# Kernel tuning notes

Measured on AMD Instinct MI355X. Metric: run time of the kernel, lower is better.

Reference implementation:

```python
import jax, jax.numpy as jnp
import numpy as np
from jax import lax

B, N, K, D = 16, 64, 20, 4096
DI, DO, H, L = 1024, 1024, 1024, 2


def setup_inputs() -> dict:
    key = jax.random.key(0)
    ks = jax.random.split(key, 16)
    s = 0.02
    x = jax.random.normal(ks[0], (B, N, K, D), dtype=jnp.float32)
    W_img = jax.random.normal(ks[1], (D, DI), dtype=jnp.float32) * s
    b_img = jnp.zeros((DI,), jnp.float32)
    W_obj = jax.random.normal(ks[2], (D, DO), dtype=jnp.float32) * s
    b_obj = jnp.zeros((DO,), jnp.float32)
    W_obj2 = jax.random.normal(ks[3], (DO, DO), dtype=jnp.float32) * s
    b_obj2 = jnp.zeros((DO,), jnp.float32)
    W_attn_h = jax.random.normal(ks[4], (H, DO), dtype=jnp.float32) * s  # hidden_lin, no bias
    W_attn_j = jax.random.normal(ks[5], (DO, 1), dtype=jnp.float32) * s  # joint_lin, no bias
    W_ih0 = jax.random.normal(ks[6], (4 * H, DI + DO), dtype=jnp.float32) * s
    W_hh0 = jax.random.normal(ks[7], (4 * H, H), dtype=jnp.float32) * s
    b0 = jnp.zeros((4 * H,), jnp.float32)  # b_ih + b_hh combined
    W_ih1 = jax.random.normal(ks[8], (4 * H, H), dtype=jnp.float32) * s
    W_hh1 = jax.random.normal(ks[9], (4 * H, H), dtype=jnp.float32) * s
    b1 = jnp.zeros((4 * H,), jnp.float32)
    W_out = jax.random.normal(ks[10], (H, 1), dtype=jnp.float32) * s
    b_out = jnp.zeros((1,), jnp.float32)
    return dict(x=x, W_img=W_img, b_img=b_img, W_obj=W_obj, b_obj=b_obj,
                W_obj2=W_obj2, b_obj2=b_obj2, W_attn_h=W_attn_h, W_attn_j=W_attn_j,
                W_ih0=W_ih0, W_hh0=W_hh0, b0=b0, W_ih1=W_ih1, W_hh1=W_hh1, b1=b1,
                W_out=W_out, b_out=b_out)


def _lstm_cell(xin, h, c, W_ih, W_hh, b):
    # PyTorch gate order: i, f, g, o
    g = xin @ W_ih.T + h @ W_hh.T + b
    i, f, gg, o = jnp.split(g, 4, axis=-1)
    c_new = jax.nn.sigmoid(f) * c + jax.nn.sigmoid(i) * jnp.tanh(gg)
    h_new = jax.nn.sigmoid(o) * jnp.tanh(c_new)
    return h_new, c_new


def reference(x, W_img, b_img, W_obj, b_obj, W_obj2, b_obj2, W_attn_h, W_attn_j,
              W_ih0, W_hh0, b0, W_ih1, W_hh1, b1, W_out, b_out):
    # obj_mask: (B,N,K-1,1)
    obj_mask = jnp.sum(x[:, :, 1:], axis=-1, keepdims=True)
    img_feat = x[:, :, 0, :] @ W_img + b_img                       # (B,N,DI)
    obj_feat = (x[:, :, 1:, :] @ W_obj + b_obj) * obj_mask          # (B,N,K-1,DO)
    a = obj_feat @ W_obj2 + b_obj2                                  # (B,N,K-1,DO)

    # move frame axis first for scan
    a_t = jnp.moveaxis(a, 1, 0)          # (N,B,K-1,DO)
    img_t = jnp.moveaxis(img_feat, 1, 0)  # (N,B,DI)
    m_t = jnp.moveaxis(obj_mask, 1, 0)    # (N,B,K-1,1)

    h0 = jnp.zeros((L, x.shape[0], H), x.dtype)
    c0 = jnp.zeros((L, x.shape[0], H), x.dtype)

    def step(carry, inp):
        h, c = carry
        a_f, img_f, m_f = inp
        # Fattn: alpha = softmax(joint_lin(tanh(hidden_lin(h_prev) + a)) * mask) over objects
        e = jnp.tanh((h[-1] @ W_attn_h)[:, None, :] + a_f)          # (B,K-1,DO)
        scores = (e @ W_attn_j) * m_f                                # (B,K-1,1)
        alphas = jax.nn.softmax(scores, axis=1)                      # over K-1
        w_obj = jnp.sum(a_f * alphas, axis=1)                        # (B,DO)
        fusion = jnp.concatenate([img_f, w_obj], axis=-1)            # (B,DI+DO)
        h1, c1 = _lstm_cell(fusion, h[0], c[0], W_ih0, W_hh0, b0)
        h2, c2 = _lstm_cell(h1, h[1], c[1], W_ih1, W_hh1, b1)
        pred = jax.nn.sigmoid(h2 @ W_out + b_out)                    # (B,1)
        return (jnp.stack([h1, h2]), jnp.stack([c1, c2])), (alphas[..., 0], pred)

    _, (all_alphas, all_preds) = lax.scan(step, (h0, c0), (a_t, img_t, m_t))
    return all_alphas, all_preds  # (N,B,K-1), (N,B,1)
```

## Files before the change

kernel.cpp:

```cpp
#include <hip/hip_runtime.h>
#include <cmath>

constexpr int B_  = 16;
constexpr int N_  = 64;
constexpr int K_  = 20;
constexpr int KM1 = 19;
constexpr int D_  = 4096;
constexpr int DO_ = 1024;
constexpr int H_  = 1024;
constexpr int G4_ = 4096;

typedef unsigned short u16;
typedef unsigned int   u32;
typedef __attribute__((ext_vector_type(8))) short bf16x8;
typedef __attribute__((ext_vector_type(4))) float f32x4;

typedef const void __attribute__((address_space(1)))* gas1_t;
typedef void __attribute__((address_space(3)))* las3_t;

static __device__ __forceinline__ void gll16(const void* g, void* l) {
  __builtin_amdgcn_global_load_lds((gas1_t)g, (las3_t)l, 16, 0, 0);
}

static __device__ __forceinline__ float sigmoidf_(float x) {
  return 1.0f / (1.0f + expf(-x));
}

static __device__ __forceinline__ u16 bf16rne(float f) {
  u32 u = __float_as_uint(f);
  return (u16)((u + 0x7fffu + ((u >> 16) & 1u)) >> 16);
}

static __device__ __forceinline__ float block_reduce_sum256(float v, float* red) {
  #pragma unroll
  for (int off = 32; off > 0; off >>= 1) v += __shfl_down(v, off);
  const int wid = threadIdx.x >> 6;
  if ((threadIdx.x & 63) == 0) red[wid] = v;
  __syncthreads();
  const float r = red[0] + red[1] + red[2] + red[3];
  __syncthreads();
  return r;
}

__global__ __launch_bounds__(256) void mask_kernel(const float* __restrict__ x,
                                                   float* __restrict__ mask) {
  const int r = blockIdx.x;
  const int g = r / KM1, kk = r - g * KM1;
  const float4* xp = (const float4*)(x + ((size_t)g * K_ + 1 + kk) * D_);
  float v = 0.f;
  #pragma unroll
  for (int it = 0; it < 4; ++it) {
    const float4 t = xp[threadIdx.x + it * 256];
    v += (t.x + t.y) + (t.z + t.w);
  }
  __shared__ float red[4];
  const float s = block_reduce_sum256(v, red);
  if (threadIdx.x == 0) mask[r] = s;
}

__global__ __launch_bounds__(256) void conv_kernel(
    const float* __restrict__ src, const int ld, const int cols,
    u16* __restrict__ oh, u16* __restrict__ ol)
{
  const int id = blockIdx.x * 256 + threadIdx.x;
  const int r = id / (cols >> 2), q = id - r * (cols >> 2);
  const float4 v = *(const float4*)(src + (size_t)r * ld + q * 4);
  const float vv[4] = {v.x, v.y, v.z, v.w};
  u16 h[4], lo[4];
  #pragma unroll
  for (int j = 0; j < 4; ++j) {
    h[j] = bf16rne(vv[j]);
    lo[j] = bf16rne(vv[j] - __uint_as_float((u32)h[j] << 16));
  }
  const size_t o = (size_t)r * cols + q * 4;
  *(ushort4*)(oh + o) = make_ushort4(h[0], h[1], h[2], h[3]);
  *(ushort4*)(ol + o) = make_ushort4(lo[0], lo[1], lo[2], lo[3]);
}

__global__ __launch_bounds__(256) void tconv_kernel(
    const float* __restrict__ src, const int R, const int C,
    u16* __restrict__ oh, u16* __restrict__ ol)
{
  __shared__ float st[64][68];
  const int t = threadIdx.x;
  const int r0 = blockIdx.y * 64, c0 = blockIdx.x * 64;
  const int lr = t >> 4, lc4 = (t & 15) * 4;
  #pragma unroll
  for (int i = 0; i < 4; ++i) {
    const float4 v = *(const float4*)(src + (size_t)(r0 + lr + 16 * i) * C + c0 + lc4);
    st[lr + 16 * i][lc4 + 0] = v.x; st[lr + 16 * i][lc4 + 1] = v.y;
    st[lr + 16 * i][lc4 + 2] = v.z; st[lr + 16 * i][lc4 + 3] = v.w;
  }
  __syncthreads();
  #pragma unroll
  for (int i = 0; i < 4; ++i) {
    const int s = t + 256 * i;
    const int c = s & 63, rq = s >> 6;
    u16 h[4], lo[4];
    #pragma unroll
    for (int j = 0; j < 4; ++j) {
      const float f = st[rq * 4 + j][c];
      h[j] = bf16rne(f);
      lo[j] = bf16rne(f - __uint_as_float((u32)h[j] << 16));
    }
    const size_t o = (size_t)(c0 + c) * R + r0 + rq * 4;
    *(ushort4*)(oh + o) = make_ushort4(h[0], h[1], h[2], h[3]);
    *(ushort4*)(ol + o) = make_ushort4(lo[0], lo[1], lo[2], lo[3]);
  }
}

__global__ __launch_bounds__(256) void bf_kernel(
    const float* __restrict__ b1, const float* __restrict__ W2, float* __restrict__ bf)
{
  const int n = blockIdx.x * 256 + threadIdx.x;
  float acc = 0.f;
  for (int j = 0; j < 1024; ++j) acc = fmaf(b1[j], W2[(size_t)j * 1024 + n], acc);
  bf[n] = acc;
}

template<int AMODE, int EPI>
__global__ __launch_bounds__(256, 2) void mfma_gemm(
    const float* __restrict__ Af,
    const u16* __restrict__ Ah, const u16* __restrict__ Al,
    const u16* __restrict__ Bh, const u16* __restrict__ Bl,
    const float* __restrict__ bias, const float* __restrict__ bias2,
    const float* __restrict__ scale,
    float* __restrict__ Cf, u16* __restrict__ Coh, u16* __restrict__ Col,
    const int Kk, const int Nn)
{
  __shared__ alignas(16) char sm[32768];
  const int t = threadIdx.x;
  const int m0 = blockIdx.x * 128, n0 = blockIdx.y * 128;
  const int w = t >> 6, l = t & 63;
  const int wm = w >> 1, wn = w & 1;

  const int srow = t >> 3;
  const int sc16 = (t & 7) * 16;

  const u16* bsrc[4]; int bdst[4];
  #pragma unroll
  for (int i = 0; i < 4; ++i) {
    const int row = srow + 32 * i;
    const int clog = sc16 ^ ((row & 7) << 4);
    const u16* base = (clog & 64) ? Bl : Bh;
    bsrc[i] = base + (size_t)(n0 + row) * Kk + ((clog & 63) >> 1);
    bdst[i] = 16384 + row * 128 + sc16;
  }

  const float* aptr[4]; int awhi[4], awlo[4];
  const u16* asrc[4]; int adst[4];
  if (AMODE == 0) {
    #pragma unroll
    for (int i = 0; i < 4; ++i) {
      const int row = srow + 32 * i;
      const int clog = sc16 ^ ((row & 7) << 4);
      const u16* base = (clog & 64) ? Al : Ah;
      asrc[i] = base + (size_t)(m0 + row) * Kk + ((clog & 63) >> 1);
      adst[i] = row * 128 + sc16;
    }
  } else {
    #pragma unroll
    for (int i = 0; i < 4; ++i) {
      const int row = srow + 32 * i;
      const int gr = m0 + row;
      size_t roff;
      if (AMODE == 1) { const int g = gr / 19, kk = gr - g * 19;
                        roff = (size_t)(g * 20 + 1 + kk) * 4096; }
      else            { roff = (size_t)gr * (20 * 4096); }
      aptr[i] = Af + roff + (t & 7) * 4;
      const int swz = (row & 7) << 4;
      awhi[i] = row * 128 + (((t & 7) * 8) ^ swz);
      awlo[i] = row * 128 + ((((t & 7) * 8) + 64) ^ swz);
    }
  }

  const int lk16 = (l >> 4) * 16;
  int aoh[4], aol[4], boh[4], bol[4];
  #pragma unroll
  for (int f = 0; f < 4; ++f) {
    const int ar = wm * 64 + f * 16 + (l & 15);
    const int sa = (ar & 7) << 4;
    aoh[f] = ar * 128 + (lk16 ^ sa);
    aol[f] = ar * 128 + ((lk16 + 64) ^ sa);
    const int br = wn * 64 + f * 16 + (l & 15);
    const int sb = (br & 7) << 4;
    boh[f] = 16384 + br * 128 + (lk16 ^ sb);
    bol[f] = 16384 + br * 128 + ((lk16 + 64) ^ sb);
  }

  f32x4 acc[4][4] = {};
  const int nk = Kk >> 5;
  for (int kt = 0; kt < nk; ++kt) {
    #pragma unroll
    for (int i = 0; i < 4; ++i) gll16(bsrc[i] + kt * 32, sm + bdst[i]);
    if (AMODE == 0) {
      #pragma unroll
      for (int i = 0; i < 4; ++i) gll16(asrc[i] + kt * 32, sm + adst[i]);
    } else {
      #pragma unroll
      for (int i = 0; i < 4; ++i) {
        const float4 v = *(const float4*)(aptr[i] + kt * 32);
        const u32 u0 = __float_as_uint(v.x), u1 = __float_as_uint(v.y);
        const u32 u2 = __float_as_uint(v.z), u3 = __float_as_uint(v.w);
        const u32 h01 = (u0 >> 16) | (u1 & 0xffff0000u);
        const u32 h23 = (u2 >> 16) | (u3 & 0xffff0000u);
        const float l0 = v.x - __uint_as_float(u0 & 0xffff0000u);
        const float l1 = v.y - __uint_as_float(u1 & 0xffff0000u);
        const float l2 = v.z - __uint_as_float(u2 & 0xffff0000u);
        const float l3 = v.w - __uint_as_float(u3 & 0xffff0000u);
        const u32 lo01 = (__float_as_uint(l0) >> 16) | (__float_as_uint(l1) & 0xffff0000u);
        const u32 lo23 = (__float_as_uint(l2) >> 16) | (__float_as_uint(l3) & 0xffff0000u);
        *(uint2*)(sm + awhi[i]) = make_uint2(h01, h23);
        *(uint2*)(sm + awlo[i]) = make_uint2(lo01, lo23);
      }
    }
    __syncthreads();

    bf16x8 ah[4], alo[4], bh[4], blo[4];
    #pragma unroll
    for (int f = 0; f < 4; ++f) {
      ah[f]  = *(const bf16x8*)(sm + aoh[f]);
      alo[f] = *(const bf16x8*)(sm + aol[f]);
      bh[f]  = *(const bf16x8*)(sm + boh[f]);
      blo[f] = *(const bf16x8*)(sm + bol[f]);
    }
    #pragma unroll
    for (int mi = 0; mi < 4; ++mi)
      #pragma unroll
      for (int ni = 0; ni < 4; ++ni) {
        acc[mi][ni] = __builtin_amdgcn_mfma_f32_16x16x32_bf16(ah[mi],  bh[ni],  acc[mi][ni], 0, 0, 0);
        acc[mi][ni] = __builtin_amdgcn_mfma_f32_16x16x32_bf16(ah[mi],  blo[ni], acc[mi][ni], 0, 0, 0);
        acc[mi][ni] = __builtin_amdgcn_mfma_f32_16x16x32_bf16(alo[mi], bh[ni],  acc[mi][ni], 0, 0, 0);
      }
    __syncthreads();
  }

  #pragma unroll
  for (int mi = 0; mi < 4; ++mi) {
    const int gr0 = m0 + wm * 64 + mi * 16 + ((l >> 4) << 2);
    #pragma unroll
    for (int ni = 0; ni < 4; ++ni) {
      const int gc = n0 + wn * 64 + ni * 16 + (l & 15);
      const float bb = bias ? bias[gc] : 0.0f;
      const float b2v = (EPI == 2) ? bias2[gc] : 0.0f;
      const f32x4 v = acc[mi][ni];
      #pragma unroll
      for (int r = 0; r < 4; ++r) {
        const int gr = gr0 + r;
        const size_t o = (size_t)gr * Nn + gc;
        if (EPI == 0) {
          Cf[o] = v[r] + bb;
        } else if (EPI == 1) {
          const float fv = v[r] + bb;
          const u16 h = bf16rne(fv);
          Coh[o] = h;
          Col[o] = bf16rne(fv - __uint_as_float((u32)h << 16));
        } else {
          Cf[o] = scale[gr] * (v[r] + bb) + b2v;
        }
      }
    }
  }
}


__global__ __launch_bounds__(256) void attn_h_kernel(
    const float* __restrict__ hB, const float* __restrict__ Wah, float* __restrict__ ahp)
{
  const int j = blockIdx.x * 256 + threadIdx.x;
  const int isl = blockIdx.y;
  float acc[B_] = {};
  for (int i0 = 0; i0 < 128; i0 += 4) {
    const int i = isl * 128 + i0;
    const float w0 = Wah[(size_t)(i + 0) * DO_ + j];
    const float w1 = Wah[(size_t)(i + 1) * DO_ + j];
    const float w2 = Wah[(size_t)(i + 2) * DO_ + j];
    const float w3 = Wah[(size_t)(i + 3) * DO_ + j];
    #pragma unroll
    for (int b = 0; b < B_; ++b) {
      const float4 hv = *(const float4*)(hB + b * H_ + i);
      acc[b] = fmaf(hv.x, w0, fmaf(hv.y, w1, fmaf(hv.z, w2, fmaf(hv.w, w3, acc[b]))));
    }
  }
  #pragma unroll
  for (int b = 0; b < B_; ++b) ahp[((size_t)isl * B_ + b) * DO_ + j] = acc[b];
}

__global__ __launch_bounds__(256) void attn_rest_kernel(
    const float* __restrict__ ahp, const float* __restrict__ a,
    const float* __restrict__ wj, const float* __restrict__ mask,
    const int n, float* __restrict__ alphas_out, float* __restrict__ wobj)
{
  const int b = blockIdx.x, tid = threadIdx.x;
  __shared__ float ahs[DO_];
  __shared__ float wjs[DO_];
  __shared__ float as_[KM1][DO_];
  __shared__ float sc[KM1 + 1];
  const size_t rowbase = (size_t)(b * N_ + n) * KM1;
  #pragma unroll
  for (int it = 0; it < 4; ++it) {
    const int j = tid + it * 256;
    float s = 0.f;
    #pragma unroll
    for (int sl = 0; sl < 8; ++sl) s += ahp[((size_t)sl * B_ + b) * DO_ + j];
    ahs[j] = s;
    wjs[j] = wj[j];
  }
  #pragma unroll
  for (int it = 0; it < 19; ++it) {
    const int i = tid + it * 256;
    const int k = i >> 8, jj = (i & 255) * 4;
    *(float4*)&as_[k][jj] = *(const float4*)(a + (rowbase + k) * DO_ + jj);
  }
  __syncthreads();
  const int w = tid >> 6, lane = tid & 63;
  for (int k = w; k < KM1; k += 4) {
    float v = 0.f;
    #pragma unroll
    for (int it = 0; it < 16; ++it) {
      const int j = lane + it * 64;
      v = fmaf(tanhf(ahs[j] + as_[k][j]), wjs[j], v);
    }
    #pragma unroll
    for (int off = 32; off > 0; off >>= 1) v += __shfl_down(v, off);
    if (lane == 0) sc[k] = v * mask[rowbase + k];
  }
  __syncthreads();
  float mx = -1e30f;
  #pragma unroll
  for (int k = 0; k < KM1; ++k) mx = fmaxf(mx, sc[k]);
  float al[KM1];
  float ssum = 0.f;
  #pragma unroll
  for (int k = 0; k < KM1; ++k) { al[k] = expf(sc[k] - mx); ssum += al[k]; }
  const float inv = 1.0f / ssum;
  if (tid < KM1) alphas_out[b * KM1 + tid] = al[tid] * inv;
  #pragma unroll
  for (int it = 0; it < 4; ++it) {
    const int j = tid + it * 256;
    float acc = 0.f;
    #pragma unroll
    for (int k = 0; k < KM1; ++k) acc = fmaf(al[k], as_[k][j], acc);
    wobj[b * DO_ + j] = acc * inv;
  }
}

__global__ __launch_bounds__(256) void gates_kernel(
    const float* __restrict__ x0, const float* __restrict__ x1,
    const float* __restrict__ W0, const int ld0, const int co0,
    const float* __restrict__ W1, const int ld1, const int co1,
    float* __restrict__ gp)
{
  constexpr int GT = 256, BK = 32, KSL = 128;
  __shared__ float Ws[BK][GT + 4];
  __shared__ float Xs[BK][20];
  const int tid = threadIdx.x;
  const int g0 = blockIdx.x * GT;
  const int ks = blockIdx.y;
  const int half = ks >> 3;
  const int koff = (ks & 7) * KSL;
  const float* X = half ? x1 : x0;
  const float* W = half ? W1 : W0;
  const int ld = half ? ld1 : ld0;
  const int co = half ? co1 : co0;
  const int tb = (tid & 7) * 2;
  const int tg = (tid >> 3) * 8;
  const float* wbase = W + (size_t)(g0 + (tid >> 3)) * ld + co + koff + (tid & 7) * 4;
  const int xb = tid & 15, xkq = (tid >> 4) * 4;

  float acc[2][8] = {};
  for (int k0 = 0; k0 < KSL; k0 += BK) {
    #pragma unroll
    for (int it = 0; it < 8; ++it) {
      const int gr = (tid >> 3) + it * 32;
      const int kq = (tid & 7) * 4;
      const float4 v = *(const float4*)(wbase + (size_t)it * 32 * ld + k0);
      Ws[kq + 0][gr] = v.x; Ws[kq + 1][gr] = v.y;
      Ws[kq + 2][gr] = v.z; Ws[kq + 3][gr] = v.w;
    }
    if (tid < 128) {
      const float4 v = *(const float4*)(X + (size_t)xb * H_ + koff + k0 + xkq);
      Xs[xkq + 0][xb] = v.x; Xs[xkq + 1][xb] = v.y;
      Xs[xkq + 2][xb] = v.z; Xs[xkq + 3][xb] = v.w;
    }
    __syncthreads();
    #pragma unroll
    for (int k = 0; k < BK; ++k) {
      float wv[8], xv[2];
      *(float4*)&wv[0] = *(const float4*)&Ws[k][tg];
      *(float4*)&wv[4] = *(const float4*)&Ws[k][tg + 4];
      *(float2*)&xv[0] = *(const float2*)&Xs[k][tb];
      #pragma unroll
      for (int bi = 0; bi < 2; ++bi)
        #pragma unroll
        for (int gi = 0; gi < 8; ++gi)
          acc[bi][gi] = fmaf(wv[gi], xv[bi], acc[bi][gi]);
    }
    __syncthreads();
  }
  float* outp = gp + (size_t)ks * B_ * G4_;
  #pragma unroll
  for (int bi = 0; bi < 2; ++bi) {
    float* op = outp + (size_t)(tb + bi) * G4_ + g0 + tg;
    *(float4*)(op)     = *(const float4*)&acc[bi][0];
    *(float4*)(op + 4) = *(const float4*)&acc[bi][4];
  }
}

__global__ __launch_bounds__(256) void cell0_kernel(
    const float* __restrict__ gp, const float* __restrict__ img_gates, const int n,
    float* __restrict__ hA, float* __restrict__ cA)
{
  const int idx = blockIdx.x * 256 + threadIdx.x;
  const int b = idx >> 10, j = idx & 1023;
  const float* ig = img_gates + ((size_t)(b * N_ + n)) * G4_;
  float gi = ig[j], gf = ig[1024 + j], gg = ig[2048 + j], go = ig[3072 + j];
  #pragma unroll
  for (int s = 0; s < 16; ++s) {
    const float* p = gp + ((size_t)s * B_ + b) * G4_;
    gi += p[j]; gf += p[1024 + j]; gg += p[2048 + j]; go += p[3072 + j];
  }
  const float c = cA[idx];
  const float cn = sigmoidf_(gf) * c + sigmoidf_(gi) * tanhf(gg);
  const float hn = sigmoidf_(go) * tanhf(cn);
  cA[idx] = cn; hA[idx] = hn;
}

__global__ __launch_bounds__(256) void cell1_kernel(
    const float* __restrict__ gp, const float* __restrict__ b1,
    const float* __restrict__ Wout,
    float* __restrict__ hB, float* __restrict__ cB, float* __restrict__ pred_acc)
{
  const int b = blockIdx.x >> 2, jq = blockIdx.x & 3, tid = threadIdx.x;
  const int j = jq * 256 + tid;
  float gi = b1[j], gf = b1[1024 + j], gg = b1[2048 + j], go = b1[3072 + j];
  #pragma unroll
  for (int s = 0; s < 16; ++s) {
    const float* p = gp + ((size_t)s * B_ + b) * G4_;
    gi += p[j]; gf += p[1024 + j]; gg += p[2048 + j]; go += p[3072 + j];
  }
  const int idx = b * H_ + j;
  const float c = cB[idx];
  const float cn = sigmoidf_(gf) * c + sigmoidf_(gi) * tanhf(gg);
  const float hn = sigmoidf_(go) * tanhf(cn);
  cB[idx] = cn; hB[idx] = hn;
  float part = hn * Wout[j];
  __shared__ float red[4];
  const float s = block_reduce_sum256(part, red);
  if (tid == 0) atomicAdd(&pred_acc[b], s);
}

__global__ __launch_bounds__(256) void pred_kernel(
    const float* __restrict__ pred_acc, const float* __restrict__ bout,
    float* __restrict__ out_pred)
{
  const float bo = bout[0];
  #pragma unroll
  for (int it = 0; it < 4; ++it) {
    const int i = threadIdx.x + it * 256;
    out_pred[i] = 1.0f / (1.0f + expf(-(pred_acc[i] + bo)));
  }
}

extern "C" void kernel_launch(void* const* d_in, const int* in_sizes, int n_in,
                              void* d_out, int out_size, void* d_ws, size_t ws_size,
                              hipStream_t stream) {
  const float* x       = (const float*)d_in[0];
  const float* W_img   = (const float*)d_in[1];
  const float* b_img   = (const float*)d_in[2];
  const float* W_obj   = (const float*)d_in[3];
  const float* b_obj   = (const float*)d_in[4];
  const float* W_obj2  = (const float*)d_in[5];
  const float* b_obj2  = (const float*)d_in[6];
  const float* W_attn_h= (const float*)d_in[7];
  const float* W_attn_j= (const float*)d_in[8];
  const float* W_ih0   = (const float*)d_in[9];
  const float* W_hh0   = (const float*)d_in[10];
  const float* b0      = (const float*)d_in[11];
  const float* W_ih1   = (const float*)d_in[12];
  const float* W_hh1   = (const float*)d_in[13];
  const float* b1      = (const float*)d_in[14];
  const float* W_out   = (const float*)d_in[15];
  const float* b_out   = (const float*)d_in[16];
  float* out = (float*)d_out;

  float* ws = (float*)d_ws;
  float* mask     = ws;
  char*  rA       = (char*)(mask + 19456);
  float* a_buf    = (float*)(rA + (size_t)19456 * 4096);
  float* ahp      = a_buf + (size_t)19456 * 1024;
  float* wobj     = ahp + 8 * B_ * DO_;
  float* hA       = wobj + B_ * DO_;
  float* cA       = hA + B_ * H_;
  float* hB       = cA + B_ * H_;
  float* cB       = hB + B_ * H_;
  float* pred_acc = cB + B_ * H_;
  float* gp       = pred_acc + N_ * B_;

  const size_t MB = 1u << 20;
  u16* W1c_h   = (u16*)(rA);
  u16* W1c_l   = (u16*)(rA +  8 * MB);
  u16* W2t_h   = (u16*)(rA + 16 * MB);
  u16* W2t_l   = (u16*)(rA + 18 * MB);
  u16* Wft_h   = (u16*)(rA + 20 * MB);
  u16* Wft_l   = (u16*)(rA + 28 * MB);
  u16* Wimgt_h = (u16*)(rA + 36 * MB);
  u16* Wimgt_l = (u16*)(rA + 44 * MB);
  u16* Wih0c_h = (u16*)(rA + 52 * MB);
  u16* Wih0c_l = (u16*)(rA + 60 * MB);
  u16* img_h   = (u16*)(rA);
  u16* img_l   = (u16*)(rA +  2 * MB);
  float* img_gates = (float*)(rA + 4 * MB);
  float* bfv   = (float*)(rA + 68 * MB);

  hipMemsetAsync(hA, 0, ((size_t)4 * B_ * H_ + N_ * B_) * sizeof(float), stream);

  mask_kernel<<<19456, 256, 0, stream>>>(x, mask);
  conv_kernel<<<4096, 256, 0, stream>>>(W_obj, 1024, 1024, W1c_h, W1c_l);
  tconv_kernel<<<dim3(16, 16), 256, 0, stream>>>(W_obj2, 1024, 1024, W2t_h, W2t_l);
  conv_kernel<<<4096, 256, 0, stream>>>(W_ih0, 2048, 1024, Wih0c_h, Wih0c_l);
  tconv_kernel<<<dim3(16, 64), 256, 0, stream>>>(W_img, 4096, 1024, Wimgt_h, Wimgt_l);
  bf_kernel<<<4, 256, 0, stream>>>(b_obj, W_obj2, bfv);

  mfma_gemm<0, 1><<<dim3(8, 32), 256, 0, stream>>>(
      nullptr, W2t_h, W2t_l, W1c_h, W1c_l,
      nullptr, nullptr, nullptr, nullptr, Wft_h, Wft_l, 1024, 4096);
  mfma_gemm<1, 2><<<dim3(152, 8), 256, 0, stream>>>(
      x, nullptr, nullptr, Wft_h, Wft_l,
      bfv, b_obj2, mask, a_buf, nullptr, nullptr, 4096, 1024);
  mfma_gemm<2, 1><<<dim3(8, 8), 256, 0, stream>>>(
      x, nullptr, nullptr, Wimgt_h, Wimgt_l,
      b_img, nullptr, nullptr, nullptr, img_h, img_l, 4096, 1024);
  mfma_gemm<0, 0><<<dim3(8, 32), 256, 0, stream>>>(
      nullptr, img_h, img_l, Wih0c_h, Wih0c_l,
      b0, nullptr, nullptr, img_gates, nullptr, nullptr, 1024, 4096);

  for (int n = 0; n < N_; ++n) {
    attn_h_kernel<<<dim3(4, 8), 256, 0, stream>>>(hB, W_attn_h, ahp);
    attn_rest_kernel<<<B_, 256, 0, stream>>>(ahp, a_buf, W_attn_j, mask, n,
                                             out + (size_t)n * (B_ * KM1), wobj);
    gates_kernel<<<dim3(16, 16), 256, 0, stream>>>(wobj, hA, W_ih0, 2048, 1024,
                                                   W_hh0, 1024, 0, gp);
    cell0_kernel<<<64, 256, 0, stream>>>(gp, img_gates, n, hA, cA);
    gates_kernel<<<dim3(16, 16), 256, 0, stream>>>(hA, hB, W_ih1, 1024, 0,
                                                   W_hh1, 1024, 0, gp);
    cell1_kernel<<<64, 256, 0, stream>>>(gp, b1, W_out, hB, cB, pred_acc + n * B_);
  }
  pred_kernel<<<1, 256, 0, stream>>>(pred_acc, b_out, out + (size_t)N_ * B_ * KM1);
}
```

Baseline: 6.116 ms.

## Move per-step recurrent GEMMs to split-bf16 MFMA with preconverted weights

```diff
diff --git a/kernel.cpp b/kernel.cpp
--- a/kernel.cpp
+++ b/kernel.cpp
@@ -30,6 +30,9 @@
   u32 u = __float_as_uint(f);
   return (u16)((u + 0x7fffu + ((u >> 16) & 1u)) >> 16);
 }
+static __device__ __forceinline__ float b2f(u16 u) {
+  return __uint_as_float((u32)u << 16);
+}
 
 static __device__ __forceinline__ float block_reduce_sum256(float v, float* red) {
   #pragma unroll
@@ -75,6 +78,25 @@
   const size_t o = (size_t)r * cols + q * 4;
   *(ushort4*)(oh + o) = make_ushort4(h[0], h[1], h[2], h[3]);
   *(ushort4*)(ol + o) = make_ushort4(lo[0], lo[1], lo[2], lo[3]);
+}
+
+__global__ __launch_bounds__(256) void conv2_kernel(
+    const float* __restrict__ src, const int sld, const int scol0,
+    u16* __restrict__ dh, u16* __restrict__ dl, const int dcol0)
+{
+  const int id = blockIdx.x * 256 + threadIdx.x;
+  const int r = id >> 8, q = id & 255;
+  const float4 v = *(const float4*)(src + (size_t)r * sld + scol0 + q * 4);
+  const float vv[4] = {v.x, v.y, v.z, v.w};
+  u16 h[4], lo[4];
+  #pragma unroll
+  for (int j = 0; j < 4; ++j) {
+    h[j] = bf16rne(vv[j]);
+    lo[j] = bf16rne(vv[j] - __uint_as_float((u32)h[j] << 16));
+  }
+  const size_t o = (size_t)r * 2048 + dcol0 + q * 4;
+  *(ushort4*)(dh + o) = make_ushort4(h[0], h[1], h[2], h[3]);
+  *(ushort4*)(dl + o) = make_ushort4(lo[0], lo[1], lo[2], lo[3]);
 }
 
 __global__ __launch_bounds__(256) void tconv_kernel(
@@ -255,71 +277,115 @@
           const u16 h = bf16rne(fv);
           Coh[o] = h;
           Col[o] = bf16rne(fv - __uint_as_float((u32)h << 16));
+        } else if (EPI == 2) {
+          Cf[o] = scale[gr] * (v[r] + bb) + b2v;
         } else {
-          Cf[o] = scale[gr] * (v[r] + bb) + b2v;
+          Coh[o] = bf16rne(v[r] + bb);
         }
       }
     }
   }
 }
 
-
-__global__ __launch_bounds__(256) void attn_h_kernel(
-    const float* __restrict__ hB, const float* __restrict__ Wah, float* __restrict__ ahp)
-{
-  const int j = blockIdx.x * 256 + threadIdx.x;
-  const int isl = blockIdx.y;
-  float acc[B_] = {};
-  for (int i0 = 0; i0 < 128; i0 += 4) {
-    const int i = isl * 128 + i0;
-    const float w0 = Wah[(size_t)(i + 0) * DO_ + j];
-    const float w1 = Wah[(size_t)(i + 1) * DO_ + j];
-    const float w2 = Wah[(size_t)(i + 2) * DO_ + j];
-    const float w3 = Wah[(size_t)(i + 3) * DO_ + j];
-    #pragma unroll
-    for (int b = 0; b < B_; ++b) {
-      const float4 hv = *(const float4*)(hB + b * H_ + i);
-      acc[b] = fmaf(hv.x, w0, fmaf(hv.y, w1, fmaf(hv.z, w2, fmaf(hv.w, w3, acc[b]))));
-    }
-  }
-  #pragma unroll
-  for (int b = 0; b < B_; ++b) ahp[((size_t)isl * B_ + b) * DO_ + j] = acc[b];
-}
+__global__ __launch_bounds__(256) void gemm16_kernel(
+    const float* __restrict__ x0, const float* __restrict__ x1, const int KH,
+    const u16* __restrict__ Wh, const u16* __restrict__ Wl, const int KT,
+    float* __restrict__ outp, const int LDO)
+{
+  __shared__ alignas(16) char sm[2048 + 8192];
+  const int t = threadIdx.x;
+  const int n0 = blockIdx.x * 64, ks = blockIdx.y;
+  const int wv = t >> 6, l = t & 63;
+
+  const u16* wsrc[2]; int wdst[2];
+  #pragma unroll
+  for (int i = 0; i < 2; ++i) {
+    const int s = t + 256 * i;
+    const int row = s >> 3, phys = (s & 7) * 16;
+    const int clog = phys ^ ((row & 7) << 4);
+    wsrc[i] = ((clog & 64) ? Wl : Wh) + (size_t)(n0 + row) * KT + ((clog & 63) >> 1);
+    wdst[i] = 2048 + s * 16;
+  }
+  const int ab = t >> 3, akq = (t & 7) * 4;
+  const int awhi = ab * 128 + ((akq * 2) ^ ((ab & 7) << 4));
+
+  const int lk16 = (l >> 4) * 16;
+  const int arow = l & 15;
+  const int aoh = arow * 128 + (lk16 ^ ((arow & 7) << 4));
+  const int wrow = wv * 16 + (l & 15);
+  const int boh = 2048 + wrow * 128 + (lk16 ^ ((wrow & 7) << 4));
+
+  f32x4 acc = {};
+  #pragma unroll
+  for (int kt = 0; kt < 4; ++kt) {
+    const int k0 = ks * 128 + kt * 32;
+    #pragma unroll
+    for (int i = 0; i < 2; ++i) gll16(wsrc[i] + k0, sm + wdst[i]);
+    if (t < 128) {
+      const float* xs = (k0 < KH) ? (x0 + (size_t)ab * 1024 + k0)
+                                  : (x1 + (size_t)ab * 1024 + (k0 - KH));
+      const float4 v = *(const float4*)(xs + akq);
+      const u32 u0 = __float_as_uint(v.x), u1 = __float_as_uint(v.y);
+      const u32 u2 = __float_as_uint(v.z), u3 = __float_as_uint(v.w);
+      const u32 h01 = (u0 >> 16) | (u1 & 0xffff0000u);
+      const u32 h23 = (u2 >> 16) | (u3 & 0xffff0000u);
+      const float l0 = v.x - __uint_as_float(u0 & 0xffff0000u);
+      const float l1 = v.y - __uint_as_float(u1 & 0xffff0000u);
+      const float l2 = v.z - __uint_as_float(u2 & 0xffff0000u);
+      const float l3 = v.w - __uint_as_float(u3 & 0xffff0000u);
+      const u32 lo01 = (__float_as_uint(l0) >> 16) | (__float_as_uint(l1) & 0xffff0000u);
+      const u32 lo23 = (__float_as_uint(l2) >> 16) | (__float_as_uint(l3) & 0xffff0000u);
+      *(uint2*)(sm + awhi) = make_uint2(h01, h23);
+      *(uint2*)(sm + (awhi ^ 64)) = make_uint2(lo01, lo23);
+    }
+    __syncthreads();
+    const bf16x8 ah = *(const bf16x8*)(sm + aoh);
+    const bf16x8 al = *(const bf16x8*)(sm + (aoh ^ 64));
+    const bf16x8 wh = *(const bf16x8*)(sm + boh);
+    const bf16x8 wl = *(const bf16x8*)(sm + (boh ^ 64));
+    acc = __builtin_amdgcn_mfma_f32_16x16x32_bf16(ah, wh, acc, 0, 0, 0);
+    acc = __builtin_amdgcn_mfma_f32_16x16x32_bf16(ah, wl, acc, 0, 0, 0);
+    acc = __builtin_amdgcn_mfma_f32_16x16x32_bf16(al, wh, acc, 0, 0, 0);
+    __syncthreads();
+  }
+  const int br = (l >> 4) * 2;
+  (void)br;
+  #pragma unroll
+  for (int r = 0; r < 4; ++r) {
+    const int b = ((l >> 4) << 2) + r;
+    outp[((size_t)ks * 16 + b) * LDO + n0 + wv * 16 + (l & 15)] = acc[r];
+  }
+}
+
 
 __global__ __launch_bounds__(256) void attn_rest_kernel(
     const float* __restrict__ ahp, const float* __restrict__ a,
     const float* __restrict__ wj, const float* __restrict__ mask,
     const int n, float* __restrict__ alphas_out, float* __restrict__ wobj)
 {
-  const int b = blockIdx.x, tid = threadIdx.x;
+  const int b = blockIdx.x, t = threadIdx.x;
   __shared__ float ahs[DO_];
   __shared__ float wjs[DO_];
-  __shared__ float as_[KM1][DO_];
   __shared__ float sc[KM1 + 1];
   const size_t rowbase = (size_t)(b * N_ + n) * KM1;
   #pragma unroll
   for (int it = 0; it < 4; ++it) {
-    const int j = tid + it * 256;
+    const int j = t + it * 256;
     float s = 0.f;
     #pragma unroll
     for (int sl = 0; sl < 8; ++sl) s += ahp[((size_t)sl * B_ + b) * DO_ + j];
     ahs[j] = s;
     wjs[j] = wj[j];
   }
-  #pragma unroll
-  for (int it = 0; it < 19; ++it) {
-    const int i = tid + it * 256;
-    const int k = i >> 8, jj = (i & 255) * 4;
-    *(float4*)&as_[k][jj] = *(const float4*)(a + (rowbase + k) * DO_ + jj);
-  }
   __syncthreads();
-  const int w = tid >> 6, lane = tid & 63;
+  const int w = t >> 6, lane = t & 63;
   for (int k = w; k < KM1; k += 4) {
+    const float* ar = a + (rowbase + k) * DO_;
     float v = 0.f;
     #pragma unroll
     for (int it = 0; it < 16; ++it) {
       const int j = lane + it * 64;
-      v = fmaf(tanhf(ahs[j] + as_[k][j]), wjs[j], v);
+      v = fmaf(tanhf(ahs[j] + ar[j]), wjs[j], v);
     }
     #pragma unroll
     for (int off = 32; off > 0; off >>= 1) v += __shfl_down(v, off);
@@ -329,92 +395,31 @@
   float mx = -1e30f;
   #pragma unroll
   for (int k = 0; k < KM1; ++k) mx = fmaxf(mx, sc[k]);
-  float al[KM1];
-  float ssum = 0.f;
+  float al[KM1], ssum = 0.f;
   #pragma unroll
   for (int k = 0; k < KM1; ++k) { al[k] = expf(sc[k] - mx); ssum += al[k]; }
   const float inv = 1.0f / ssum;
-  if (tid < KM1) alphas_out[b * KM1 + tid] = al[tid] * inv;
+  if (t < KM1) alphas_out[b * KM1 + t] = al[t] * inv;
   #pragma unroll
   for (int it = 0; it < 4; ++it) {
-    const int j = tid + it * 256;
+    const int j = t + it * 256;
     float acc = 0.f;
     #pragma unroll
-    for (int k = 0; k < KM1; ++k) acc = fmaf(al[k], as_[k][j], acc);
+    for (int k = 0; k < KM1; ++k)
+      acc = fmaf(al[k], a[(rowbase + k) * DO_ + j], acc);
     wobj[b * DO_ + j] = acc * inv;
   }
 }
 
-__global__ __launch_bounds__(256) void gates_kernel(
-    const float* __restrict__ x0, const float* __restrict__ x1,
-    const float* __restrict__ W0, const int ld0, const int co0,
-    const float* __restrict__ W1, const int ld1, const int co1,
-    float* __restrict__ gp)
-{
-  constexpr int GT = 256, BK = 32, KSL = 128;
-  __shared__ float Ws[BK][GT + 4];
-  __shared__ float Xs[BK][20];
-  const int tid = threadIdx.x;
-  const int g0 = blockIdx.x * GT;
-  const int ks = blockIdx.y;
-  const int half = ks >> 3;
-  const int koff = (ks & 7) * KSL;
-  const float* X = half ? x1 : x0;
-  const float* W = half ? W1 : W0;
-  const int ld = half ? ld1 : ld0;
-  const int co = half ? co1 : co0;
-  const int tb = (tid & 7) * 2;
-  const int tg = (tid >> 3) * 8;
-  const float* wbase = W + (size_t)(g0 + (tid >> 3)) * ld + co + koff + (tid & 7) * 4;
-  const int xb = tid & 15, xkq = (tid >> 4) * 4;
-
-  float acc[2][8] = {};
-  for (int k0 = 0; k0 < KSL; k0 += BK) {
-    #pragma unroll
-    for (int it = 0; it < 8; ++it) {
-      const int gr = (tid >> 3) + it * 32;
-      const int kq = (tid & 7) * 4;
-      const float4 v = *(const float4*)(wbase + (size_t)it * 32 * ld + k0);
-      Ws[kq + 0][gr] = v.x; Ws[kq + 1][gr] = v.y;
-      Ws[kq + 2][gr] = v.z; Ws[kq + 3][gr] = v.w;
-    }
-    if (tid < 128) {
-      const float4 v = *(const float4*)(X + (size_t)xb * H_ + koff + k0 + xkq);
-      Xs[xkq + 0][xb] = v.x; Xs[xkq + 1][xb] = v.y;
-      Xs[xkq + 2][xb] = v.z; Xs[xkq + 3][xb] = v.w;
-    }
-    __syncthreads();
-    #pragma unroll
-    for (int k = 0; k < BK; ++k) {
-      float wv[8], xv[2];
-      *(float4*)&wv[0] = *(const float4*)&Ws[k][tg];
-      *(float4*)&wv[4] = *(const float4*)&Ws[k][tg + 4];
-      *(float2*)&xv[0] = *(const float2*)&Xs[k][tb];
-      #pragma unroll
-      for (int bi = 0; bi < 2; ++bi)
-        #pragma unroll
-        for (int gi = 0; gi < 8; ++gi)
-          acc[bi][gi] = fmaf(wv[gi], xv[bi], acc[bi][gi]);
-    }
-    __syncthreads();
-  }
-  float* outp = gp + (size_t)ks * B_ * G4_;
-  #pragma unroll
-  for (int bi = 0; bi < 2; ++bi) {
-    float* op = outp + (size_t)(tb + bi) * G4_ + g0 + tg;
-    *(float4*)(op)     = *(const float4*)&acc[bi][0];
-    *(float4*)(op + 4) = *(const float4*)&acc[bi][4];
-  }
-}
-
 __global__ __launch_bounds__(256) void cell0_kernel(
-    const float* __restrict__ gp, const float* __restrict__ img_gates, const int n,
+    const float* __restrict__ gp, const u16* __restrict__ igh, const int n,
     float* __restrict__ hA, float* __restrict__ cA)
 {
   const int idx = blockIdx.x * 256 + threadIdx.x;
   const int b = idx >> 10, j = idx & 1023;
-  const float* ig = img_gates + ((size_t)(b * N_ + n)) * G4_;
-  float gi = ig[j], gf = ig[1024 + j], gg = ig[2048 + j], go = ig[3072 + j];
+  const u16* ig = igh + ((size_t)(b * N_ + n)) * G4_;
+  float gi = b2f(ig[j]), gf = b2f(ig[1024 + j]);
+  float gg = b2f(ig[2048 + j]), go = b2f(ig[3072 + j]);
   #pragma unroll
   for (int s = 0; s < 16; ++s) {
     const float* p = gp + ((size_t)s * B_ + b) * G4_;
@@ -508,10 +513,16 @@
   u16* Wimgt_l = (u16*)(rA + 44 * MB);
   u16* Wih0c_h = (u16*)(rA + 52 * MB);
   u16* Wih0c_l = (u16*)(rA + 60 * MB);
-  u16* img_h   = (u16*)(rA);
-  u16* img_l   = (u16*)(rA +  2 * MB);
-  float* img_gates = (float*)(rA + 4 * MB);
   float* bfv   = (float*)(rA + 68 * MB);
+  u16* img_h   = (u16*)(rA + 20 * MB);
+  u16* img_l   = (u16*)(rA + 22 * MB);
+  u16* igh     = (u16*)(rA);
+  u16* Wg0h    = (u16*)(rA +  8 * MB);
+  u16* Wg0l    = (u16*)(rA + 24 * MB);
+  u16* Wg1h    = (u16*)(rA + 40 * MB);
+  u16* Wg1l    = (u16*)(rA + 56 * MB);
+  u16* Waht_h  = (u16*)(rA + 72 * MB);
+  u16* Waht_l  = (u16*)(rA + 74 * MB);
 
   hipMemsetAsync(hA, 0, ((size_t)4 * B_ * H_ + N_ * B_) * sizeof(float), stream);
 
@@ -531,19 +542,26 @@
   mfma_gemm<2, 1><<<dim3(8, 8), 256, 0, stream>>>(
       x, nullptr, nullptr, Wimgt_h, Wimgt_l,
       b_img, nullptr, nullptr, nullptr, img_h, img_l, 4096, 1024);
-  mfma_gemm<0, 0><<<dim3(8, 32), 256, 0, stream>>>(
+  mfma_gemm<0, 3><<<dim3(8, 32), 256, 0, stream>>>(
       nullptr, img_h, img_l, Wih0c_h, Wih0c_l,
-      b0, nullptr, nullptr, img_gates, nullptr, nullptr, 1024, 4096);
+      b0, nullptr, nullptr, nullptr, igh, nullptr, 1024, 4096);
+
+  tconv_kernel<<<dim3(16, 16), 256, 0, stream>>>(W_attn_h, 1024, 1024, Waht_h, Waht_l);
+  conv2_kernel<<<4096, 256, 0, stream>>>(W_ih0, 2048, 1024, Wg0h, Wg0l, 0);
+  conv2_kernel<<<4096, 256, 0, stream>>>(W_hh0, 1024, 0,    Wg0h, Wg0l, 1024);
+  conv2_kernel<<<4096, 256, 0, stream>>>(W_ih1, 1024, 0,    Wg1h, Wg1l, 0);
+  conv2_kernel<<<4096, 256, 0, stream>>>(W_hh1, 1024, 0,    Wg1h, Wg1l, 1024);
 
   for (int n = 0; n < N_; ++n) {
-    attn_h_kernel<<<dim3(4, 8), 256, 0, stream>>>(hB, W_attn_h, ahp);
+    gemm16_kernel<<<dim3(16, 8), 256, 0, stream>>>(
+        hB, hB, 1024, Waht_h, Waht_l, 1024, ahp, 1024);
     attn_rest_kernel<<<B_, 256, 0, stream>>>(ahp, a_buf, W_attn_j, mask, n,
                                              out + (size_t)n * (B_ * KM1), wobj);
-    gates_kernel<<<dim3(16, 16), 256, 0, stream>>>(wobj, hA, W_ih0, 2048, 1024,
-                                                   W_hh0, 1024, 0, gp);
-    cell0_kernel<<<64, 256, 0, stream>>>(gp, img_gates, n, hA, cA);
-    gates_kernel<<<dim3(16, 16), 256, 0, stream>>>(hA, hB, W_ih1, 1024, 0,
-                                                   W_hh1, 1024, 0, gp);
+    gemm16_kernel<<<dim3(64, 16), 256, 0, stream>>>(
+        wobj, hA, 1024, Wg0h, Wg0l, 2048, gp, 4096);
+    cell0_kernel<<<64, 256, 0, stream>>>(gp, igh, n, hA, cA);
+    gemm16_kernel<<<dim3(64, 16), 256, 0, stream>>>(
+        hA, hB, 1024, Wg1h, Wg1l, 2048, gp, 4096);
     cell1_kernel<<<64, 256, 0, stream>>>(gp, b1, W_out, hB, cB, pred_acc + n * B_);
   }
   pred_kernel<<<1, 256, 0, stream>>>(pred_acc, b_out, out + (size_t)N_ * B_ * KM1);
```

Measured after the change: 6.342 ms. 3.7% more time.
